# Performance work log

Hardware: AMD Instinct MI355X
Metric: run time of the kernel (lower is better)

## Reference

```python
import jax, jax.numpy as jnp
import numpy as np
from jax import lax

SIGMA = 1.0
TRUNCATE = 4.0  # skimage.filters.gaussian default


def _gauss_kernel(sigma, truncate=TRUNCATE):
    radius = int(truncate * sigma + 0.5)
    t = np.arange(-radius, radius + 1, dtype=np.float32)
    k = np.exp(-0.5 * (t / sigma) ** 2)
    k = k / k.sum()
    return jnp.asarray(k), radius


def setup_inputs() -> dict:
    key = jax.random.key(0)
    x = jax.random.uniform(key, (128, 1, 512, 512), dtype=jnp.float32)
    return {"x": x}


def _blur(x, sigma=SIGMA):
    # x: [B, 1, H, W] -> squeeze channel like the torch module, blur, return [B, H, W]
    k, r = _gauss_kernel(sigma)
    K = 2 * r + 1
    # 'nearest' boundary mode of skimage == edge padding
    xp = jnp.pad(x, ((0, 0), (0, 0), (r, r), (r, r)), mode="edge")
    kh = k.reshape(1, 1, K, 1).astype(x.dtype)  # vertical pass
    kw = k.reshape(1, 1, 1, K).astype(x.dtype)  # horizontal pass
    dn = lax.conv_dimension_numbers(xp.shape, kh.shape, ("NCHW", "OIHW", "NCHW"))
    y = lax.conv_general_dilated(xp, kh, (1, 1), "VALID", dimension_numbers=dn)
    y = lax.conv_general_dilated(y, kw, (1, 1), "VALID", dimension_numbers=dn)
    return y[:, 0]  # [B, H, W], matching x_i.squeeze() per-sample output


def reference(x):
    return _blur(x)
```

## Files before the change

kernel.cpp:

```cpp
#include <hip/hip_runtime.h>

namespace {

constexpr int R     = 4;
constexpr int TSX   = 64;
constexpr int TSY   = 32;
constexpr int RAWH  = TSY + 2 * R;
constexpr int RSTR  = 76;
constexpr int HSTR  = 68;
constexpr int IMG_H = 512;
constexpr int IMG_W = 512;
constexpr int NMAIN = RAWH * (TSX / 4);
constexpr int NHALO = RAWH * 2;
constexpr int NHP   = RAWH * (TSX / 4);

__device__ __forceinline__ int clampi(int v, int lo, int hi) {
    return v < lo ? lo : (v > hi ? hi : v);
}

__global__ __launch_bounds__(256)
void gauss_blur_kernel(const float* __restrict__ in, float* __restrict__ out) {
    const float KW[9] = {
        1.3383062e-4f, 4.4318616e-3f, 5.3990966e-2f, 2.4197144e-1f,
        3.9894347e-1f, 2.4197144e-1f, 5.3990966e-2f, 4.4318616e-3f,
        1.3383062e-4f};

    __shared__ float s_raw[RAWH * RSTR];
    __shared__ float s_h  [RAWH * HSTR];

    const int tid = threadIdx.x;
    const int b   = blockIdx.z;
    const int ty0 = blockIdx.y * TSY;
    const int tx0 = blockIdx.x * TSX;

    const float* __restrict__ inb = in + (size_t)b * IMG_H * IMG_W;

    const bool interior = (tx0 - R >= 0) && (tx0 + TSX - R + 4 + 3 < IMG_W);

    if (interior) {
        for (int i = tid; i < NMAIN; i += 256) {
            const int r = i >> 4, c = i & 15;
            const int gy = clampi(ty0 - R + r, 0, IMG_H - 1);
            float4 v = *reinterpret_cast<const float4*>(
                inb + (size_t)gy * IMG_W + (tx0 - R + 4 * c));
            *reinterpret_cast<float4*>(&s_raw[r * RSTR + 4 * c]) = v;
        }
        if (tid < NHALO) {
            const int r = tid >> 1, h = tid & 1;
            const int gy = clampi(ty0 - R + r, 0, IMG_H - 1);
            float4 v = *reinterpret_cast<const float4*>(
                inb + (size_t)gy * IMG_W + (tx0 + TSX - R + 4 * h));
            *reinterpret_cast<float4*>(&s_raw[r * RSTR + TSX + 4 * h]) = v;
        }
    } else {
        for (int i = tid; i < NMAIN + NHALO; i += 256) {
            int r, cc;
            if (i < NMAIN) { r = i >> 4; cc = 4 * (i & 15); }
            else           { int k = i - NMAIN; r = k >> 1; cc = TSX + 4 * (k & 1); }
            const int gy = clampi(ty0 - R + r, 0, IMG_H - 1);
            const float* rp = inb + (size_t)gy * IMG_W;
            const int gx = tx0 - R + cc;
            float4 v;
            v.x = rp[clampi(gx + 0, 0, IMG_W - 1)];
            v.y = rp[clampi(gx + 1, 0, IMG_W - 1)];
            v.z = rp[clampi(gx + 2, 0, IMG_W - 1)];
            v.w = rp[clampi(gx + 3, 0, IMG_W - 1)];
            *reinterpret_cast<float4*>(&s_raw[r * RSTR + cc]) = v;
        }
    }
    __syncthreads();

    for (int i = tid; i < NHP; i += 256) {
        const int r = i >> 4, j = i & 15;
        const float* rp = &s_raw[r * RSTR + 4 * j];
        float4 a  = *reinterpret_cast<const float4*>(rp);
        float4 bq = *reinterpret_cast<const float4*>(rp + 4);
        float4 cq = *reinterpret_cast<const float4*>(rp + 8);
        float w[12] = {a.x, a.y, a.z, a.w, bq.x, bq.y, bq.z, bq.w,
                       cq.x, cq.y, cq.z, cq.w};
        float a0 = 0.f, a1 = 0.f, a2 = 0.f, a3 = 0.f;
        #pragma unroll
        for (int t = 0; t < 9; ++t) {
            a0 = fmaf(KW[t], w[t + 0], a0);
            a1 = fmaf(KW[t], w[t + 1], a1);
            a2 = fmaf(KW[t], w[t + 2], a2);
            a3 = fmaf(KW[t], w[t + 3], a3);
        }
        float4 o = {a0, a1, a2, a3};
        *reinterpret_cast<float4*>(&s_h[r * HSTR + 4 * j]) = o;
    }
    __syncthreads();

    const int px  = tid & 15;
    const int py  = tid >> 4;
    const int lx  = 4 * px;
    const int oy0 = 2 * py;

    float4 acc0 = {0.f, 0.f, 0.f, 0.f};
    float4 acc1 = {0.f, 0.f, 0.f, 0.f};
    #pragma unroll
    for (int t = 0; t < 10; ++t) {
        float4 h = *reinterpret_cast<const float4*>(&s_h[(oy0 + t) * HSTR + lx]);
        if (t < 9) {
            acc0.x = fmaf(KW[t], h.x, acc0.x);
            acc0.y = fmaf(KW[t], h.y, acc0.y);
            acc0.z = fmaf(KW[t], h.z, acc0.z);
            acc0.w = fmaf(KW[t], h.w, acc0.w);
        }
        if (t >= 1) {
            acc1.x = fmaf(KW[t - 1], h.x, acc1.x);
            acc1.y = fmaf(KW[t - 1], h.y, acc1.y);
            acc1.z = fmaf(KW[t - 1], h.z, acc1.z);
            acc1.w = fmaf(KW[t - 1], h.w, acc1.w);
        }
    }

    float* __restrict__ outb = out + (size_t)b * IMG_H * IMG_W;
    *reinterpret_cast<float4*>(&outb[(size_t)(ty0 + oy0) * IMG_W + tx0 + lx]) = acc0;
    *reinterpret_cast<float4*>(&outb[(size_t)(ty0 + oy0 + 1) * IMG_W + tx0 + lx]) = acc1;
}

}

extern "C" void kernel_launch(void* const* d_in, const int* in_sizes, int n_in,
                              void* d_out, int out_size, void* d_ws, size_t ws_size,
                              hipStream_t stream) {
    const float* x = (const float*)d_in[0];
    float* out = (float*)d_out;

    const int batch = in_sizes[0] / (IMG_H * IMG_W);

    dim3 grid(IMG_W / TSX, IMG_H / TSY, batch);
    gauss_blur_kernel<<<grid, 256, 0, stream>>>(x, out);
}
```

Measured before the change: 64.34 us.

## Make blocks own full-height column strips and do horizontal pass from registers

Each block now handles a 64-wide column strip over the whole image height, looping over 32-row steps, rather than one 64x32 tile. The raw-input shared buffer is gone: each thread loads three overlapping float4s straight from global memory, handles edge clamping with an in-register replicate, and writes the horizontal-pass result into shared memory. The goal is less shared-memory traffic and fewer blocks, at the cost of reading each input row about three times from global/L1, re-reading the halo rows at every step, and a 1024-block grid with an in-kernel serial loop that may hurt occupancy and latency hiding.

```diff
diff --git a/kernel.cpp b/kernel.cpp
--- a/kernel.cpp
+++ b/kernel.cpp
@@ -2,17 +2,13 @@
 
 namespace {
 
-constexpr int R     = 4;
+constexpr int IMG   = 512;
 constexpr int TSX   = 64;
-constexpr int TSY   = 32;
-constexpr int RAWH  = TSY + 2 * R;
-constexpr int RSTR  = 76;
+constexpr int STEP  = 32;
+constexpr int HR    = STEP + 8;
 constexpr int HSTR  = 68;
-constexpr int IMG_H = 512;
-constexpr int IMG_W = 512;
-constexpr int NMAIN = RAWH * (TSX / 4);
-constexpr int NHALO = RAWH * 2;
-constexpr int NHP   = RAWH * (TSX / 4);
+constexpr int NSTEP = IMG / STEP;
+constexpr int NITEM = HR * 16;
 
 __device__ __forceinline__ int clampi(int v, int lo, int hi) {
     return v < lo ? lo : (v > hi ? hi : v);
@@ -25,99 +21,91 @@
         3.9894347e-1f, 2.4197144e-1f, 5.3990966e-2f, 4.4318616e-3f,
         1.3383062e-4f};
 
-    __shared__ float s_raw[RAWH * RSTR];
-    __shared__ float s_h  [RAWH * HSTR];
+    __shared__ float s_h[HR * HSTR];
 
     const int tid = threadIdx.x;
-    const int b   = blockIdx.z;
-    const int ty0 = blockIdx.y * TSY;
-    const int tx0 = blockIdx.x * TSX;
+    const int bx  = blockIdx.x;
+    const int b   = blockIdx.y;
+    const int tx0 = bx * TSX;
+    const bool blkL = (bx == 0);
+    const bool blkR = (bx == (IMG / TSX) - 1);
 
-    const float* __restrict__ inb = in + (size_t)b * IMG_H * IMG_W;
-
-    const bool interior = (tx0 - R >= 0) && (tx0 + TSX - R + 4 + 3 < IMG_W);
-
-    if (interior) {
-        for (int i = tid; i < NMAIN; i += 256) {
-            const int r = i >> 4, c = i & 15;
-            const int gy = clampi(ty0 - R + r, 0, IMG_H - 1);
-            float4 v = *reinterpret_cast<const float4*>(
-                inb + (size_t)gy * IMG_W + (tx0 - R + 4 * c));
-            *reinterpret_cast<float4*>(&s_raw[r * RSTR + 4 * c]) = v;
-        }
-        if (tid < NHALO) {
-            const int r = tid >> 1, h = tid & 1;
-            const int gy = clampi(ty0 - R + r, 0, IMG_H - 1);
-            float4 v = *reinterpret_cast<const float4*>(
-                inb + (size_t)gy * IMG_W + (tx0 + TSX - R + 4 * h));
-            *reinterpret_cast<float4*>(&s_raw[r * RSTR + TSX + 4 * h]) = v;
-        }
-    } else {
-        for (int i = tid; i < NMAIN + NHALO; i += 256) {
-            int r, cc;
-            if (i < NMAIN) { r = i >> 4; cc = 4 * (i & 15); }
-            else           { int k = i - NMAIN; r = k >> 1; cc = TSX + 4 * (k & 1); }
-            const int gy = clampi(ty0 - R + r, 0, IMG_H - 1);
-            const float* rp = inb + (size_t)gy * IMG_W;
-            const int gx = tx0 - R + cc;
-            float4 v;
-            v.x = rp[clampi(gx + 0, 0, IMG_W - 1)];
-            v.y = rp[clampi(gx + 1, 0, IMG_W - 1)];
-            v.z = rp[clampi(gx + 2, 0, IMG_W - 1)];
-            v.w = rp[clampi(gx + 3, 0, IMG_W - 1)];
-            *reinterpret_cast<float4*>(&s_raw[r * RSTR + cc]) = v;
-        }
-    }
-    __syncthreads();
-
-    for (int i = tid; i < NHP; i += 256) {
-        const int r = i >> 4, j = i & 15;
-        const float* rp = &s_raw[r * RSTR + 4 * j];
-        float4 a  = *reinterpret_cast<const float4*>(rp);
-        float4 bq = *reinterpret_cast<const float4*>(rp + 4);
-        float4 cq = *reinterpret_cast<const float4*>(rp + 8);
-        float w[12] = {a.x, a.y, a.z, a.w, bq.x, bq.y, bq.z, bq.w,
-                       cq.x, cq.y, cq.z, cq.w};
-        float a0 = 0.f, a1 = 0.f, a2 = 0.f, a3 = 0.f;
-        #pragma unroll
-        for (int t = 0; t < 9; ++t) {
-            a0 = fmaf(KW[t], w[t + 0], a0);
-            a1 = fmaf(KW[t], w[t + 1], a1);
-            a2 = fmaf(KW[t], w[t + 2], a2);
-            a3 = fmaf(KW[t], w[t + 3], a3);
-        }
-        float4 o = {a0, a1, a2, a3};
-        *reinterpret_cast<float4*>(&s_h[r * HSTR + 4 * j]) = o;
-    }
-    __syncthreads();
+    const float* __restrict__ inb  = in  + (size_t)b * IMG * IMG;
+    float* __restrict__       outb = out + (size_t)b * IMG * IMG;
 
     const int px  = tid & 15;
     const int py  = tid >> 4;
     const int lx  = 4 * px;
     const int oy0 = 2 * py;
 
-    float4 acc0 = {0.f, 0.f, 0.f, 0.f};
-    float4 acc1 = {0.f, 0.f, 0.f, 0.f};
-    #pragma unroll
-    for (int t = 0; t < 10; ++t) {
-        float4 h = *reinterpret_cast<const float4*>(&s_h[(oy0 + t) * HSTR + lx]);
-        if (t < 9) {
-            acc0.x = fmaf(KW[t], h.x, acc0.x);
-            acc0.y = fmaf(KW[t], h.y, acc0.y);
-            acc0.z = fmaf(KW[t], h.z, acc0.z);
-            acc0.w = fmaf(KW[t], h.w, acc0.w);
+    #pragma unroll 1
+    for (int k = 0; k < NSTEP; ++k) {
+        const int ybase = STEP * k - 4;
+
+        float4 L[3][3];
+        #pragma unroll
+        for (int it = 0; it < 3; ++it) {
+            const int i = tid + 256 * it;
+            if (i < NITEM) {
+                const int r   = i >> 4;
+                const int j   = i & 15;
+                const int gy  = clampi(ybase + r, 0, IMG - 1);
+                const int gxm = tx0 - 4 + 4 * j;
+                const float* rp = inb + (size_t)gy * IMG;
+                L[it][0] = *reinterpret_cast<const float4*>(rp + clampi(gxm,     0, IMG - 4));
+                L[it][1] = *reinterpret_cast<const float4*>(rp + clampi(gxm + 4, 0, IMG - 4));
+                L[it][2] = *reinterpret_cast<const float4*>(rp + clampi(gxm + 8, 0, IMG - 4));
+            }
         }
-        if (t >= 1) {
-            acc1.x = fmaf(KW[t - 1], h.x, acc1.x);
-            acc1.y = fmaf(KW[t - 1], h.y, acc1.y);
-            acc1.z = fmaf(KW[t - 1], h.z, acc1.z);
-            acc1.w = fmaf(KW[t - 1], h.w, acc1.w);
+        #pragma unroll
+        for (int it = 0; it < 3; ++it) {
+            const int i = tid + 256 * it;
+            if (i < NITEM) {
+                const int r = i >> 4;
+                const int j = i & 15;
+                float4 lf = L[it][0], md = L[it][1], rt = L[it][2];
+                if (blkL && j == 0)  { const float e = lf.x; lf = make_float4(e, e, e, e); }
+                if (blkR && j == 15) { const float e = rt.w; rt = make_float4(e, e, e, e); }
+                const float w[12] = {lf.x, lf.y, lf.z, lf.w,
+                                     md.x, md.y, md.z, md.w,
+                                     rt.x, rt.y, rt.z, rt.w};
+                float a0 = 0.f, a1 = 0.f, a2 = 0.f, a3 = 0.f;
+                #pragma unroll
+                for (int t = 0; t < 9; ++t) {
+                    a0 = fmaf(KW[t], w[t + 0], a0);
+                    a1 = fmaf(KW[t], w[t + 1], a1);
+                    a2 = fmaf(KW[t], w[t + 2], a2);
+                    a3 = fmaf(KW[t], w[t + 3], a3);
+                }
+                float4 o = {a0, a1, a2, a3};
+                *reinterpret_cast<float4*>(&s_h[r * HSTR + 4 * j]) = o;
+            }
         }
+        __syncthreads();
+
+        float4 acc0 = {0.f, 0.f, 0.f, 0.f};
+        float4 acc1 = {0.f, 0.f, 0.f, 0.f};
+        #pragma unroll
+        for (int t = 0; t < 10; ++t) {
+            float4 h = *reinterpret_cast<const float4*>(&s_h[(oy0 + t) * HSTR + lx]);
+            if (t < 9) {
+                acc0.x = fmaf(KW[t], h.x, acc0.x);
+                acc0.y = fmaf(KW[t], h.y, acc0.y);
+                acc0.z = fmaf(KW[t], h.z, acc0.z);
+                acc0.w = fmaf(KW[t], h.w, acc0.w);
+            }
+            if (t >= 1) {
+                acc1.x = fmaf(KW[t - 1], h.x, acc1.x);
+                acc1.y = fmaf(KW[t - 1], h.y, acc1.y);
+                acc1.z = fmaf(KW[t - 1], h.z, acc1.z);
+                acc1.w = fmaf(KW[t - 1], h.w, acc1.w);
+            }
+        }
+        const int y = STEP * k + oy0;
+        *reinterpret_cast<float4*>(&outb[(size_t)y * IMG + tx0 + lx])       = acc0;
+        *reinterpret_cast<float4*>(&outb[(size_t)(y + 1) * IMG + tx0 + lx]) = acc1;
+        __syncthreads();
     }
-
-    float* __restrict__ outb = out + (size_t)b * IMG_H * IMG_W;
-    *reinterpret_cast<float4*>(&outb[(size_t)(ty0 + oy0) * IMG_W + tx0 + lx]) = acc0;
-    *reinterpret_cast<float4*>(&outb[(size_t)(ty0 + oy0 + 1) * IMG_W + tx0 + lx]) = acc1;
 }
 
 }
@@ -128,8 +116,8 @@
     const float* x = (const float*)d_in[0];
     float* out = (float*)d_out;
 
-    const int batch = in_sizes[0] / (IMG_H * IMG_W);
+    const int batch = in_sizes[0] / (IMG * IMG);
 
-    dim3 grid(IMG_W / TSX, IMG_H / TSY, batch);
+    dim3 grid(IMG / TSX, batch);
     gauss_blur_kernel<<<grid, 256, 0, stream>>>(x, out);
 }
```

Result: no change. 64.95 us (+0.9%).
